# Kernel optimization log

Hardware: AMD Instinct MI355X
Metric: run time of the kernel (lower is better)

Reference implementation:

```python
import jax, jax.numpy as jnp
import numpy as np

D_K = 128  # d_model / h


def setup_inputs() -> dict:
    key = jax.random.key(0)
    ks = jax.random.split(key, 7)
    N, d_model, h, d_k = 8192, 2048, 16, D_K
    q = jax.random.normal(ks[0], (N, d_model), dtype=jnp.float32)
    # per-head projection weights, RandomNormal(stddev=1.0) in source
    Wq = jax.random.normal(ks[1], (h, d_model, d_k), dtype=jnp.float32)
    Wk = jax.random.normal(ks[2], (h, d_model, d_k), dtype=jnp.float32)
    Wv = jax.random.normal(ks[3], (h, d_model, d_k), dtype=jnp.float32)
    # learned key/value rows and output proj, keras 'uniform' init (+-0.05)
    k_param = jax.random.uniform(ks[4], (1, d_model), dtype=jnp.float32, minval=-0.05, maxval=0.05)
    v_param = jax.random.uniform(ks[5], (1, d_model), dtype=jnp.float32, minval=-0.05, maxval=0.05)
    Wo = jax.random.uniform(ks[6], (d_model, d_model), dtype=jnp.float32, minval=-0.05, maxval=0.05)
    return {"q": q, "Wq": Wq, "Wk": Wk, "Wv": Wv, "k_param": k_param, "v_param": v_param, "Wo": Wo}


def reference(q, Wq, Wk, Wv, k_param, v_param, Wo):
    d_k = Wq.shape[-1]
    scale = jnp.sqrt(jnp.float32(d_k))
    # batched per-head projections: (h, N, d_k), (h, 1, d_k)
    q_proj = jnp.einsum('nd,hdk->hnk', q, Wq)
    k_proj = jnp.einsum('od,hdk->hok', k_param, Wk)
    v_proj = jnp.einsum('od,hdk->hok', v_param, Wv)
    scores = jnp.einsum('hnk,hok->hno', q_proj, k_proj) / scale  # (h, N, 1)
    weights = jax.nn.softmax(scores, axis=-1)  # size-1 softmax -> ones (faithful)
    head_out = jnp.einsum('hno,hok->hnk', weights, v_proj)  # (h, N, d_k)
    N = q.shape[0]
    concat = jnp.transpose(head_out, (1, 0, 2)).reshape(N, -1)  # (N, h*d_k)
    return concat @ Wo
```

## Files before the change

kernel.cpp:

```cpp
#include <hip/hip_runtime.h>


#define NROWS 8192
#define DM    2048
#define H     16
#define DK    128
#define NCH   32
#define DCH   64

__global__ __launch_bounds__(128) void k_vproj(const float* __restrict__ Wv,
                                               const float* __restrict__ vparam,
                                               float* __restrict__ part1) {
    const int c = blockIdx.x;
    const int h = blockIdx.y;
    const int k = threadIdx.x;
    const float* wp = Wv + (size_t)h * DM * DK + (size_t)c * DCH * DK + k;
    const float* vq = vparam + c * DCH;
    float acc = 0.f;
#pragma unroll 8
    for (int d = 0; d < DCH; ++d) {
        acc += vq[d] * wp[(size_t)d * DK];
    }
    part1[c * (H * DK) + h * DK + k] = acc;
}

__global__ __launch_bounds__(256) void k_rowproj(const float* __restrict__ part1,
                                                 const float* __restrict__ Wo,
                                                 float* __restrict__ part2) {
    const int mb = blockIdx.x;
    const int jc = blockIdx.y;
    const int t  = threadIdx.x;
    __shared__ float vp[64];
    if (t < 64) {
        const int j = jc * 64 + t;
        float s = 0.f;
#pragma unroll
        for (int c = 0; c < NCH; ++c) s += part1[c * DM + j];
        vp[t] = s;
    }
    __syncthreads();
    const int m = mb * 256 + t;
    const float* wo = Wo + (size_t)(jc * 64) * DM + m;
    float acc = 0.f;
#pragma unroll 8
    for (int jj = 0; jj < 64; ++jj) acc += vp[jj] * wo[(size_t)jj * DM];
    part2[jc * DM + m] = acc;
}

__global__ __launch_bounds__(256) void k_bcast(const float* __restrict__ part2,
                                               float* __restrict__ out) {
    const int cs = blockIdx.x;
    const int rg = blockIdx.y;
    const int t  = threadIdx.x;
    const float4* p4 = (const float4*)(part2) + cs * 256 + t;
    float4 acc = {0.f, 0.f, 0.f, 0.f};
#pragma unroll
    for (int c = 0; c < NCH; ++c) {
        const float4 v = p4[c * (DM / 4)];
        acc.x += v.x; acc.y += v.y; acc.z += v.z; acc.w += v.w;
    }
    float4* out4 = (float4*)out + (size_t)(rg * 32) * (DM / 4) + cs * 256 + t;
#pragma unroll
    for (int r = 0; r < 32; ++r) {
        out4[(size_t)r * (DM / 4)] = acc;
    }
}

extern "C" void kernel_launch(void* const* d_in, const int* in_sizes, int n_in,
                              void* d_out, int out_size, void* d_ws, size_t ws_size,
                              hipStream_t stream) {
    const float* Wv     = (const float*)d_in[3];
    const float* vparam = (const float*)d_in[5];
    const float* Wo     = (const float*)d_in[6];
    float* out = (float*)d_out;

    float* part1 = (float*)d_ws;
    float* part2 = part1 + NCH * DM;

    k_vproj  <<<dim3(NCH, H), 128, 0, stream>>>(Wv, vparam, part1);
    k_rowproj<<<dim3(8, NCH), 256, 0, stream>>>(part1, Wo, part2);
    k_bcast  <<<dim3(2, 256), 256, 0, stream>>>(part2, out);
}
```

Before: 29.69 us.

## Replace partial-sum buffers with atomicAdd reductions and finer split-K grids

Both reduction stages now accumulate directly into a single vector with float atomicAdd, replacing the 32 partial rows per stage. The split-K grids are widened (64 chunks for the V projection, 128 chunks for the Wo product), and a memset zeroes the workspace beforehand. This removes the partial-row reads in the second and third kernels and spreads the weight reads over more blocks. In exchange it adds a memset launch and atomic contention, and summation order is no longer deterministic.

Result: slower. 33.24 us (+12.0%).

```diff
diff --git a/kernel.cpp b/kernel.cpp
--- a/kernel.cpp
+++ b/kernel.cpp
@@ -1,68 +1,52 @@
 #include <hip/hip_runtime.h>
 
 
-#define NROWS 8192
-#define DM    2048
-#define H     16
-#define DK    128
-#define NCH   32
-#define DCH   64
+#define DM 2048
+#define H  16
+#define DK 128
 
 __global__ __launch_bounds__(128) void k_vproj(const float* __restrict__ Wv,
                                                const float* __restrict__ vparam,
-                                               float* __restrict__ part1) {
+                                               float* __restrict__ vp) {
     const int c = blockIdx.x;
     const int h = blockIdx.y;
     const int k = threadIdx.x;
-    const float* wp = Wv + (size_t)h * DM * DK + (size_t)c * DCH * DK + k;
-    const float* vq = vparam + c * DCH;
+    const float* wp = Wv + ((size_t)h * DM + (size_t)c * 32) * DK + k;
+    const float* vq = vparam + c * 32;
     float acc = 0.f;
-#pragma unroll 8
-    for (int d = 0; d < DCH; ++d) {
+#pragma unroll
+    for (int d = 0; d < 32; ++d) {
         acc += vq[d] * wp[(size_t)d * DK];
     }
-    part1[c * (H * DK) + h * DK + k] = acc;
+    atomicAdd(&vp[h * DK + k], acc);
 }
 
-__global__ __launch_bounds__(256) void k_rowproj(const float* __restrict__ part1,
+__global__ __launch_bounds__(256) void k_rowproj(const float* __restrict__ vp,
                                                  const float* __restrict__ Wo,
-                                                 float* __restrict__ part2) {
+                                                 float* __restrict__ r) {
     const int mb = blockIdx.x;
     const int jc = blockIdx.y;
     const int t  = threadIdx.x;
-    __shared__ float vp[64];
-    if (t < 64) {
-        const int j = jc * 64 + t;
-        float s = 0.f;
+    const int m  = mb * 256 + t;
+    const float* wo = Wo + (size_t)(jc * 16) * DM + m;
+    float acc = 0.f;
 #pragma unroll
-        for (int c = 0; c < NCH; ++c) s += part1[c * DM + j];
-        vp[t] = s;
+    for (int jl = 0; jl < 16; ++jl) {
+        acc += vp[jc * 16 + jl] * wo[(size_t)jl * DM];
     }
-    __syncthreads();
-    const int m = mb * 256 + t;
-    const float* wo = Wo + (size_t)(jc * 64) * DM + m;
-    float acc = 0.f;
-#pragma unroll 8
-    for (int jj = 0; jj < 64; ++jj) acc += vp[jj] * wo[(size_t)jj * DM];
-    part2[jc * DM + m] = acc;
+    atomicAdd(&r[m], acc);
 }
 
-__global__ __launch_bounds__(256) void k_bcast(const float* __restrict__ part2,
+__global__ __launch_bounds__(256) void k_bcast(const float* __restrict__ r,
                                                float* __restrict__ out) {
     const int cs = blockIdx.x;
     const int rg = blockIdx.y;
     const int t  = threadIdx.x;
-    const float4* p4 = (const float4*)(part2) + cs * 256 + t;
-    float4 acc = {0.f, 0.f, 0.f, 0.f};
-#pragma unroll
-    for (int c = 0; c < NCH; ++c) {
-        const float4 v = p4[c * (DM / 4)];
-        acc.x += v.x; acc.y += v.y; acc.z += v.z; acc.w += v.w;
-    }
+    const float4 v = ((const float4*)r)[cs * 256 + t];
     float4* out4 = (float4*)out + (size_t)(rg * 32) * (DM / 4) + cs * 256 + t;
 #pragma unroll
-    for (int r = 0; r < 32; ++r) {
-        out4[(size_t)r * (DM / 4)] = acc;
+    for (int n = 0; n < 32; ++n) {
+        out4[(size_t)n * (DM / 4)] = v;
     }
 }
 
@@ -74,10 +58,11 @@
     const float* Wo     = (const float*)d_in[6];
     float* out = (float*)d_out;
 
-    float* part1 = (float*)d_ws;
-    float* part2 = part1 + NCH * DM;
+    float* vp = (float*)d_ws;
+    float* r  = vp + DM;
 
-    k_vproj  <<<dim3(NCH, H), 128, 0, stream>>>(Wv, vparam, part1);
-    k_rowproj<<<dim3(8, NCH), 256, 0, stream>>>(part1, Wo, part2);
-    k_bcast  <<<dim3(2, 256), 256, 0, stream>>>(part2, out);
+    hipMemsetAsync(d_ws, 0, 2 * DM * sizeof(float), stream);
+    k_vproj  <<<dim3(64, H),   128, 0, stream>>>(Wv, vparam, vp);
+    k_rowproj<<<dim3(8, 128),  256, 0, stream>>>(vp, Wo, r);
+    k_bcast  <<<dim3(2, 256),  256, 0, stream>>>(r, out);
 }
```
